# Optimization experiments

Hardware: AMD Instinct MI355X
Metric: run time of the kernel (lower is better)

## Reference

```python
import jax, jax.numpy as jnp
import numpy as np

H = 16      # n_head
DK = 64     # d_k = n_feat // n_head
EPS = 1e-5  # nn.LayerNorm default eps


def _layernorm(x, gamma, beta):
    # LayerNorm over the last (d_k) dim, matching nn.LayerNorm(d_k)
    mu = jnp.mean(x, axis=-1, keepdims=True)
    var = jnp.mean(jnp.square(x - mu), axis=-1, keepdims=True)
    return (x - mu) * jax.lax.rsqrt(var + EPS) * gamma + beta


def setup_inputs() -> dict:
    key = jax.random.key(0)
    ks = jax.random.split(key, 10)
    B, T, D = 4, 1024, 1024
    s = 0.02
    inp = {
        "query": jax.random.normal(ks[0], (B, T, D), dtype=jnp.float32),
        "key":   jax.random.normal(ks[1], (B, T, D), dtype=jnp.float32),
        "value": jax.random.normal(ks[2], (B, T, D), dtype=jnp.float32),
        "mask":  jax.random.randint(ks[3], (B, T, T), 0, 2).astype(bool),
        # projection weights (torch nn.Linear: y = x @ W.T + b)
        "Wq": jax.random.normal(ks[4], (D, D), dtype=jnp.float32) * s,
        "bq": jnp.zeros((D,), dtype=jnp.float32),
        "Wk": jax.random.normal(ks[5], (D, D), dtype=jnp.float32) * s,
        "bk": jnp.zeros((D,), dtype=jnp.float32),
        "Wv": jax.random.normal(ks[6], (D, D), dtype=jnp.float32) * s,
        "bv": jnp.zeros((D,), dtype=jnp.float32),
        "Wo": jax.random.normal(ks[7], (D, D), dtype=jnp.float32) * s,
        "bo": jnp.zeros((D,), dtype=jnp.float32),
        # per-head LayerNorm params over d_k
        "q_gamma": jnp.ones((DK,), dtype=jnp.float32),
        "q_beta":  jnp.zeros((DK,), dtype=jnp.float32),
        "k_gamma": jnp.ones((DK,), dtype=jnp.float32),
        "k_beta":  jnp.zeros((DK,), dtype=jnp.float32),
    }
    return inp


def reference(query, key, value, mask, Wq, bq, Wk, bk, Wv, bv, Wo, bo,
              q_gamma, q_beta, k_gamma, k_beta):
    B, Tq, D = query.shape
    Tk = key.shape[1]
    # forward_qkv: project, split heads, QK-LayerNorm
    q = (query @ Wq.T + bq).reshape(B, Tq, H, DK)
    k = (key   @ Wk.T + bk).reshape(B, Tk, H, DK)
    q = _layernorm(q, q_gamma, q_beta).transpose(0, 2, 1, 3)  # (B,H,Tq,dk)
    k = _layernorm(k, k_gamma, k_beta).transpose(0, 2, 1, 3)  # (B,H,Tk,dk)
    v = (value @ Wv.T + bv).reshape(B, Tk, H, DK).transpose(0, 2, 1, 3)
    # scores scaled by sqrt(d_k)
    scores = jnp.einsum('bhqd,bhkd->bhqk', q, k) / jnp.sqrt(jnp.float32(DK))
    m = mask[:, None]  # (B,1,Tq,Tk) broadcast over heads
    scores = jnp.where(m, jnp.float32(-10000.0), scores)
    attn = jax.nn.softmax(scores, axis=-1)
    attn = jnp.where(m, jnp.float32(0.0), attn)
    # dropout is identity (p=0.0, eval)
    x = jnp.einsum('bhqk,bhkd->bhqd', attn, v)
    x = x.transpose(0, 2, 1, 3).reshape(B, Tq, H * DK)
    return x @ Wo.T + bo
```

## Files before the change

kernel.cpp:

```cpp
#include <hip/hip_runtime.h>
#include <cstdint>
#include <cstddef>

typedef _Float16 half8  __attribute__((ext_vector_type(8)));
typedef _Float16 half4v __attribute__((ext_vector_type(4)));
typedef float    f32x4  __attribute__((ext_vector_type(4)));

__device__ __forceinline__ f32x4 fzero4() {
  f32x4 v; v[0] = v[1] = v[2] = v[3] = 0.0f; return v;
}

__device__ __forceinline__ void gload16(const void* g, void* l) {
  __builtin_amdgcn_global_load_lds(
      (const __attribute__((address_space(1))) unsigned int*)g,
      (__attribute__((address_space(3))) unsigned int*)l, 16, 0, 0);
}

#define MFMA(a, b, c) __builtin_amdgcn_mfma_f32_16x16x32_f16(a, b, c, 0, 0, 0)
#define EXP2(x) __builtin_amdgcn_exp2f(x)

__device__ __forceinline__ float row16_sum(float x) {
#define STEP_(N)                                                         \
  {                                                                      \
    int t_ = __builtin_amdgcn_update_dpp(0, __float_as_int(x), 0x120 | N, \
                                         0xf, 0xf, true);                \
    x = x + __int_as_float(t_);                                          \
  }
  STEP_(8) STEP_(4) STEP_(2) STEP_(1)
#undef STEP_
  return x;
}

struct PrepArgs {
  const float* src[7];
  _Float16*    dst[7];
  const int*   mask;
  unsigned long long* mbits;
};

__global__ __launch_bounds__(256) void prep_kernel(PrepArgs a) {
  const int z = blockIdx.y;
  const int nthr = gridDim.x * blockDim.x;
  const int t0 = blockIdx.x * blockDim.x + threadIdx.x;
  if (z < 3) {
    const float4* __restrict__ s = (const float4*)a.src[z];
    half4v* __restrict__ d = (half4v*)a.dst[z];
    float4 v[8];
#pragma unroll
    for (int k = 0; k < 8; ++k) v[k] = s[t0 + k * nthr];
#pragma unroll
    for (int k = 0; k < 8; ++k) {
      half4v h;
      h[0] = (_Float16)v[k].x; h[1] = (_Float16)v[k].y;
      h[2] = (_Float16)v[k].z; h[3] = (_Float16)v[k].w;
      d[t0 + k * nthr] = h;
    }
  } else if (z < 7) {
    const float4* __restrict__ s = (const float4*)a.src[z];
    half4v* __restrict__ d = (half4v*)a.dst[z];
    float4 v[2];
#pragma unroll
    for (int k = 0; k < 2; ++k) v[k] = s[t0 + k * nthr];
#pragma unroll
    for (int k = 0; k < 2; ++k) {
      half4v h;
      h[0] = (_Float16)v[k].x; h[1] = (_Float16)v[k].y;
      h[2] = (_Float16)v[k].z; h[3] = (_Float16)v[k].w;
      d[t0 + k * nthr] = h;
    }
  } else {
    const int* __restrict__ src = a.mask;
    const unsigned char* __restrict__ s8 = (const unsigned char*)src;
    unsigned long long* __restrict__ dst = a.mbits;
    const int lane = threadIdx.x & 63;
    unsigned probe = 0;
#pragma unroll
    for (int e = 0; e < 16; ++e) probe |= s8[4 * (lane * 16 + e) + 1];
    const bool isbool = __any(probe != 0);

    const int gw = blockIdx.x * 4 + (threadIdx.x >> 6);
    for (int ii = 0; ii < 32; ii += 8) {
      int mv[8];
#pragma unroll
      for (int k = 0; k < 8; ++k) {
        const int word = gw * 32 + ii + k;
        const int t = word & 1023;
        const int kw = (word >> 10) & 15;
        const int b = word >> 14;
        const size_t idx = ((size_t)(b * 1024 + t)) * 1024 + kw * 64 + lane;
        mv[k] = isbool ? (int)s8[idx] : src[idx];
      }
#pragma unroll
      for (int k = 0; k < 8; ++k) {
        unsigned long long bal = __ballot(mv[k] != 0);
        if (lane == 0) dst[gw * 32 + ii + k] = bal;
      }
    }
  }
}

#define SM_SCALE 0.18033688011112042f

__global__ __launch_bounds__(256) void proj_kernel(
    const _Float16* __restrict__ q16, const _Float16* __restrict__ k16,
    const _Float16* __restrict__ v16, const _Float16* __restrict__ w16,
    const float* __restrict__ bq, const float* __restrict__ bk,
    const float* __restrict__ bv,
    const float* __restrict__ qg, const float* __restrict__ qbt,
    const float* __restrict__ kg, const float* __restrict__ kbt,
    _Float16* __restrict__ Qln, _Float16* __restrict__ Kln,
    _Float16* __restrict__ VT) {
  __shared__ _Float16 As[128 * 64];
  __shared__ _Float16 Bs[128 * 64];

  const int tid = threadIdx.x;
  const int w = tid >> 6, lane = tid & 63, g = lane >> 4, l15 = lane & 15;
  const int flat = blockIdx.x;
  const int swz = (flat & 7) * 96 + (flat >> 3);
  const int bn = swz & 7;
  const int bm = (swz >> 3) & 31;
  const int z = swz >> 8;

  const _Float16* A = (z == 0) ? q16 : ((z == 1) ? k16 : v16);
  const _Float16* W = w16 + (size_t)z * (1024 * 1024);
  const float* bias = (z == 0) ? bq : ((z == 1) ? bk : bv);

  const int wr = w >> 1, wc = w & 1;
  const int srow = (w << 3) + (lane >> 3);
  const int csw = ((lane & 7) ^ (lane >> 3)) << 3;
  const int rsw = (l15 & 7) << 3;

  f32x4 acc[4][4];
#pragma unroll
  for (int i = 0; i < 4; ++i)
#pragma unroll
    for (int j = 0; j < 4; ++j) acc[i][j] = fzero4();

#define PROJ_STAGE(KT)                                                      \
  _Pragma("unroll") for (int r = 0; r < 4; ++r) {                           \
    const int row = r * 32 + srow;                                          \
    gload16(A + (size_t)(bm * 128 + row) * 1024 + (KT)*64 + csw,            \
            &As[(r * 32 + (w << 3)) * 64]);                                 \
    gload16(W + (size_t)(bn * 128 + row) * 1024 + (KT)*64 + csw,            \
            &Bs[(r * 32 + (w << 3)) * 64]);                                 \
  }

#define PROJ_COMP()                                                         \
  _Pragma("unroll") for (int kk = 0; kk < 2; ++kk) {                        \
    half8 a[4], b[4];                                                       \
    _Pragma("unroll") for (int mi = 0; mi < 4; ++mi) a[mi] =                \
        *(const half8*)&As[(wr * 64 + mi * 16 + l15) * 64 +                 \
                           ((kk * 32 + g * 8) ^ rsw)];                      \
    _Pragma("unroll") for (int nj = 0; nj < 4; ++nj) b[nj] =                \
        *(const half8*)&Bs[(wc * 64 + nj * 16 + l15) * 64 +                 \
                           ((kk * 32 + g * 8) ^ rsw)];                      \
    __builtin_amdgcn_s_setprio(1);                                          \
    _Pragma("unroll") for (int mi = 0; mi < 4; ++mi)                        \
        _Pragma("unroll") for (int nj = 0; nj < 4; ++nj) acc[mi][nj] =      \
            MFMA(a[mi], b[nj], acc[mi][nj]);                                \
    __builtin_amdgcn_s_setprio(0);                                          \
  }

  for (int kt = 0; kt < 16; ++kt) {
    PROJ_STAGE(kt)
    asm volatile("s_waitcnt vmcnt(0)" ::: "memory");
    __syncthreads();
    PROJ_COMP()
    __syncthreads();
  }
#undef PROJ_COMP
#undef PROJ_STAGE

  const int colbase = bn * 128 + wc * 64;
  const int h = colbase >> 6;
  const int rowbase = bm * 128 + wr * 64;

  float biasv[4];
#pragma unroll
  for (int nj = 0; nj < 4; ++nj) biasv[nj] = bias[colbase + nj * 16 + l15];

  if (z < 2) {
    const float* gamma = (z == 0) ? qg : kg;
    const float* beta = (z == 0) ? qbt : kbt;
    const float sc = (z == 0) ? SM_SCALE : 1.0f;
    _Float16* dst = (z == 0) ? Qln : Kln;
    float gam[4], bet[4];
#pragma unroll
    for (int nj = 0; nj < 4; ++nj) {
      gam[nj] = gamma[nj * 16 + l15] * sc;
      bet[nj] = beta[nj * 16 + l15] * sc;
    }
#pragma unroll
    for (int mi = 0; mi < 4; ++mi) {
#pragma unroll
      for (int j = 0; j < 4; ++j) {
        float vals[4], s = 0.f, s2 = 0.f;
#pragma unroll
        for (int nj = 0; nj < 4; ++nj) {
          float v = acc[mi][nj][j] + biasv[nj];
          vals[nj] = v; s += v; s2 += v * v;
        }
        s = row16_sum(s);
        s2 = row16_sum(s2);
        const float mu = s * (1.0f / 64.0f);
        const float var = s2 * (1.0f / 64.0f) - mu * mu;
        const float rs = rsqrtf(var + 1e-5f);
        const int r = rowbase + mi * 16 + g * 4 + j;
        const int b = r >> 10, t = r & 1023;
        _Float16* drow = dst + ((size_t)((b * 16 + h) * 1024 + t)) * 64;
#pragma unroll
        for (int nj = 0; nj < 4; ++nj)
          drow[nj * 16 + l15] =
              (_Float16)((vals[nj] - mu) * rs * gam[nj] + bet[nj]);
      }
    }
  } else {
#pragma unroll
    for (int mi = 0; mi < 4; ++mi) {
      const int r0 = rowbase + mi * 16 + g * 4;
      const int b = r0 >> 10, t0 = r0 & 1023;
#pragma unroll
      for (int nj = 0; nj < 4; ++nj) {
        const int dk = nj * 16 + l15;
        half4v pk;
#pragma unroll
        for (int j = 0; j < 4; ++j)
          pk[j] = (_Float16)(acc[mi][nj][j] + biasv[nj]);
        *(half4v*)&VT[((size_t)((b * 16 + h) * 64 + dk)) * 1024 + t0] = pk;
      }
    }
  }
}

#define PSTR 76

__global__ __launch_bounds__(512) void attn_kernel(
    const _Float16* __restrict__ Qln, const _Float16* __restrict__ Kln,
    const _Float16* __restrict__ VT,
    const unsigned long long* __restrict__ mbits, _Float16* __restrict__ X) {
  __shared__ _Float16 PQ[128 * PSTR];
  __shared__ _Float16 Ks[2][64 * 64];
  __shared__ _Float16 Vs[2][64 * 64];
  __shared__ unsigned long long Mb[2][128];

  const int tid = threadIdx.x;
  const int w = tid >> 6, lane = tid & 63, g = lane >> 4, l15 = lane & 15;
  const int qt = blockIdx.y;
  const int bh = blockIdx.x;
  const int b = bh >> 4, h = bh & 15;

  const int lr8 = lane >> 3;
  const int csw = ((lane & 7) ^ lr8) << 3;

  const _Float16* Qb = Qln + (size_t)bh * 65536;
  const _Float16* Kb = Kln + (size_t)bh * 65536;
  const _Float16* Vb = VT + (size_t)bh * 65536;
  const unsigned long long* mbb = mbits + (size_t)b * 16384 + qt * 128;

  gload16(Qb + (size_t)(qt * 128 + w * 16 + lr8) * 64 + csw, &PQ[(w * 16) * 64]);
  gload16(Qb + (size_t)(qt * 128 + w * 16 + 8 + lr8) * 64 + csw,
          &PQ[(w * 16 + 8) * 64]);
  gload16(Kb + (size_t)(w * 8 + lr8) * 64 + csw, &Ks[0][(w * 8) * 64]);
  gload16(Vb + (size_t)(w * 8 + lr8) * 1024 + csw, &Vs[0][(w * 8) * 64]);
  if (w == 0) gload16(mbb + lane * 2, &Mb[0][0]);
  asm volatile("s_waitcnt vmcnt(0)" ::: "memory");
  __syncthreads();

  const int rsw = (l15 & 7) << 3;
  half8 qf[2];
#pragma unroll
  for (int kk = 0; kk < 2; ++kk)
    qf[kk] = *(const half8*)&PQ[(w * 16 + l15) * 64 + ((kk * 32 + g * 8) ^ rsw)];
  asm volatile("s_waitcnt lgkmcnt(0)" ::: "memory");
  __syncthreads();

  f32x4 o[4];
  float lsum[4];
#pragma unroll
  for (int dn = 0; dn < 4; ++dn) o[dn] = fzero4();
#pragma unroll
  for (int j = 0; j < 4; ++j) lsum[j] = 0.f;

#define ATTN_TILE(KT, CUR, NXT, PF)                                          \
  {                                                                          \
    if (PF) {                                                                \
      gload16(Kb + (size_t)(((KT) + 1) * 64 + w * 8 + lr8) * 64 + csw,       \
              &Ks[NXT][(w * 8) * 64]);                                       \
      gload16(Vb + (size_t)(w * 8 + lr8) * 1024 + ((KT) + 1) * 64 + csw,     \
              &Vs[NXT][(w * 8) * 64]);                                       \
      if (w == 0)                                                            \
        gload16(mbb + (size_t)((KT) + 1) * 1024 + lane * 2, &Mb[NXT][0]);    \
    }                                                                        \
    f32x4 s[4];                                                              \
    _Pragma("unroll") for (int nj = 0; nj < 4; ++nj) s[nj] = fzero4();       \
    _Pragma("unroll") for (int kk = 0; kk < 2; ++kk) {                       \
      half8 qv = qf[kk];                                                     \
      __builtin_amdgcn_s_setprio(1);                                         \
      _Pragma("unroll") for (int nj = 0; nj < 4; ++nj) {                     \
        half8 kf = *(const half8*)&Ks[CUR][(nj * 16 + l15) * 64 +            \
                                          ((kk * 32 + g * 8) ^ rsw)];        \
        s[nj] = MFMA(qv, kf, s[nj]);                                         \
      }                                                                      \
      __builtin_amdgcn_s_setprio(0);                                         \
    }                                                                        \
    _Pragma("unroll") for (int j = 0; j < 4; ++j) {                          \
      const int lrow = w * 16 + g * 4 + j;                                   \
      const unsigned long long mw = Mb[CUR][lrow];                           \
      const unsigned lo = (unsigned)mw, hi = (unsigned)(mw >> 32);           \
      const float p0 = ((lo >> l15) & 1) ? 0.f : EXP2(s[0][j]);              \
      const float p1 = ((lo >> (l15 + 16)) & 1) ? 0.f : EXP2(s[1][j]);       \
      const float p2 = ((hi >> l15) & 1) ? 0.f : EXP2(s[2][j]);              \
      const float p3 = ((hi >> (l15 + 16)) & 1) ? 0.f : EXP2(s[3][j]);       \
      PQ[lrow * PSTR + 0 + l15] = (_Float16)p0;                              \
      PQ[lrow * PSTR + 16 + l15] = (_Float16)p1;                             \
      PQ[lrow * PSTR + 32 + l15] = (_Float16)p2;                             \
      PQ[lrow * PSTR + 48 + l15] = (_Float16)p3;                             \
      lsum[j] += (p0 + p1) + (p2 + p3);                                      \
    }                                                                        \
    _Pragma("unroll") for (int kk = 0; kk < 2; ++kk) {                       \
      half8 pa = *(const half8*)&PQ[(w * 16 + l15) * PSTR + kk * 32 + g * 8];\
      __builtin_amdgcn_s_setprio(1);                                         \
      _Pragma("unroll") for (int dn = 0; dn < 4; ++dn) {                     \
        half8 vf = *(const half8*)&Vs[CUR][(dn * 16 + l15) * 64 +            \
                                           ((kk * 32 + g * 8) ^ rsw)];       \
        o[dn] = MFMA(pa, vf, o[dn]);                                         \
      }                                                                      \
      __builtin_amdgcn_s_setprio(0);                                         \
    }                                                                        \
    if (PF) {                                                                \
      asm volatile("s_waitcnt vmcnt(0)" ::: "memory");                       \
      __syncthreads();                                                       \
    }                                                                        \
  }

  for (int kt = 0; kt < 16; kt += 2) {
    ATTN_TILE(kt, 0, 1, true);
    ATTN_TILE(kt + 1, 1, 0, (kt + 1) < 15);
  }
#undef ATTN_TILE

#pragma unroll
  for (int j = 0; j < 4; ++j) {
    const int t = qt * 128 + w * 16 + g * 4 + j;
    const float inv = 1.0f / row16_sum(lsum[j]);
    _Float16* xrow = X + ((size_t)(b * 1024 + t)) * 1024 + h * 64;
#pragma unroll
    for (int dn = 0; dn < 4; ++dn)
      xrow[dn * 16 + l15] = (_Float16)(o[dn][j] * inv);
  }
}

__global__ __launch_bounds__(256) void ogemm_kernel(
    const _Float16* __restrict__ Xin, const _Float16* __restrict__ Wo16,
    const float* __restrict__ bo, float* __restrict__ out) {
  __shared__ _Float16 As[2][128 * 64];
  __shared__ _Float16 Bs[2][64 * 64];

  const int tid = threadIdx.x;
  const int w = tid >> 6, lane = tid & 63, g = lane >> 4, l15 = lane & 15;
  const int flat = blockIdx.x;
  const int swz = (flat & 7) * 64 + (flat >> 3);
  const int bn = swz & 15;
  const int bm = swz >> 4;
  const int wr = w >> 1, wc = w & 1;
  const int srow = (w << 3) + (lane >> 3);
  const int lr8 = lane >> 3;
  const int csw = ((lane & 7) ^ lr8) << 3;
  const int rsw = (l15 & 7) << 3;

  f32x4 acc[4][2];
#pragma unroll
  for (int i = 0; i < 4; ++i)
#pragma unroll
    for (int j = 0; j < 2; ++j) acc[i][j] = fzero4();

#define OG_STAGE(KT, BUF)                                                   \
  {                                                                         \
    _Pragma("unroll") for (int r = 0; r < 4; ++r) {                         \
      gload16(Xin + (size_t)(bm * 128 + r * 32 + srow) * 1024 + (KT)*64 +   \
                  csw,                                                      \
              &As[BUF][(r * 32 + (w << 3)) * 64]);                          \
    }                                                                       \
    _Pragma("unroll") for (int c = 0; c < 2; ++c) {                         \
      gload16(Wo16 + (size_t)(bn * 64 + w * 16 + c * 8 + lr8) * 1024 +      \
                  (KT)*64 + csw,                                            \
              &Bs[BUF][(w * 16 + c * 8) * 64]);                             \
    }                                                                       \
  }

#define OG_TILE(KT, CUR, NXT, PF)                                           \
  {                                                                         \
    if (PF) { OG_STAGE((KT) + 1, NXT) }                                     \
    _Pragma("unroll") for (int kk = 0; kk < 2; ++kk) {                      \
      half8 a[4], b[2];                                                     \
      _Pragma("unroll") for (int mi = 0; mi < 4; ++mi) a[mi] =              \
          *(const half8*)&As[CUR][(wr * 64 + mi * 16 + l15) * 64 +          \
                                  ((kk * 32 + g * 8) ^ rsw)];               \
      _Pragma("unroll") for (int nj = 0; nj < 2; ++nj) b[nj] =              \
          *(const half8*)&Bs[CUR][(wc * 32 + nj * 16 + l15) * 64 +          \
                                  ((kk * 32 + g * 8) ^ rsw)];               \
      __builtin_amdgcn_s_setprio(1);                                        \
      _Pragma("unroll") for (int mi = 0; mi < 4; ++mi)                      \
          _Pragma("unroll") for (int nj = 0; nj < 2; ++nj) acc[mi][nj] =    \
              MFMA(a[mi], b[nj], acc[mi][nj]);                              \
      __builtin_amdgcn_s_setprio(0);                                        \
    }                                                                       \
    if (PF) {                                                               \
      asm volatile("s_waitcnt vmcnt(0)" ::: "memory");                      \
      __syncthreads();                                                      \
    }                                                                       \
  }

  OG_STAGE(0, 0)
  asm volatile("s_waitcnt vmcnt(0)" ::: "memory");
  __syncthreads();
  for (int kt = 0; kt < 16; kt += 2) {
    OG_TILE(kt, 0, 1, true);
    OG_TILE(kt + 1, 1, 0, (kt + 1) < 15);
  }
#undef OG_TILE
#undef OG_STAGE

  const int colbase = bn * 64 + wc * 32;
  const int rowbase = bm * 128 + wr * 64;
  float biasv[2];
#pragma unroll
  for (int nj = 0; nj < 2; ++nj) biasv[nj] = bo[colbase + nj * 16 + l15];
#pragma unroll
  for (int mi = 0; mi < 4; ++mi)
#pragma unroll
    for (int nj = 0; nj < 2; ++nj)
#pragma unroll
      for (int j = 0; j < 4; ++j) {
        const int r = rowbase + mi * 16 + g * 4 + j;
        out[(size_t)r * 1024 + colbase + nj * 16 + l15] =
            acc[mi][nj][j] + biasv[nj];
      }
}

extern "C" void kernel_launch(void* const* d_in, const int* in_sizes, int n_in,
                              void* d_out, int out_size, void* d_ws,
                              size_t ws_size, hipStream_t stream) {
  const float* query = (const float*)d_in[0];
  const float* key = (const float*)d_in[1];
  const float* value = (const float*)d_in[2];
  const int* mask = (const int*)d_in[3];
  const float* Wq = (const float*)d_in[4];
  const float* bq = (const float*)d_in[5];
  const float* Wk = (const float*)d_in[6];
  const float* bk = (const float*)d_in[7];
  const float* Wv = (const float*)d_in[8];
  const float* bv = (const float*)d_in[9];
  const float* Wo = (const float*)d_in[10];
  const float* bo = (const float*)d_in[11];
  const float* qg = (const float*)d_in[12];
  const float* qb = (const float*)d_in[13];
  const float* kg = (const float*)d_in[14];
  const float* kb = (const float*)d_in[15];
  float* out = (float*)d_out;

  const size_t M4 = (size_t)4 * 1024 * 1024;
  const size_t M1 = (size_t)1024 * 1024;
  _Float16* q16 = (_Float16*)d_ws;
  _Float16* k16 = q16 + M4;
  _Float16* v16 = k16 + M4;
  _Float16* w16 = v16 + M4;
  _Float16* Qln = w16 + M4;
  _Float16* Kln = Qln + M4;
  _Float16* VTp = Kln + M4;
  _Float16* X = q16;
  unsigned long long* mbits = (unsigned long long*)(VTp + M4);

  PrepArgs pa;
  pa.src[0] = query; pa.src[1] = key; pa.src[2] = value;
  pa.src[3] = Wq; pa.src[4] = Wk; pa.src[5] = Wv; pa.src[6] = Wo;
  pa.dst[0] = q16; pa.dst[1] = k16; pa.dst[2] = v16;
  pa.dst[3] = w16; pa.dst[4] = w16 + M1; pa.dst[5] = w16 + 2 * M1;
  pa.dst[6] = w16 + 3 * M1;
  pa.mask = mask;
  pa.mbits = mbits;

  prep_kernel<<<dim3(512, 8), 256, 0, stream>>>(pa);
  proj_kernel<<<dim3(768), 256, 0, stream>>>(
      q16, k16, v16, w16, bq, bk, bv, qg, qb, kg, kb, Qln, Kln, VTp);
  attn_kernel<<<dim3(64, 8), 512, 0, stream>>>(Qln, Kln, VTp, mbits, X);
  ogemm_kernel<<<dim3(512), 256, 0, stream>>>(X, w16 + 3 * M1, bo, out);
}
```

Before: 116.2 us.

## Repack mask bitmask with int4 loads and interleaved per-row bit layout

The mask-packing path now reads the int32 mask with 16-byte vector loads and emits four ballot words per 256-column group, which interleaves column bits (lane*4+c) in the packed layout. The attention kernel changes its mask staging to match: it loads four 64-bit words per row once every four key tiles into a larger double-buffered LDS array and decodes bits with a new index formula. This is meant to make the mask-packing reads coalesced and cheaper, in exchange for more LDS space for mask words and more index arithmetic in the softmax loop.

```diff
diff --git a/kernel.cpp b/kernel.cpp
--- a/kernel.cpp
+++ b/kernel.cpp
@@ -78,22 +78,38 @@
     for (int e = 0; e < 16; ++e) probe |= s8[4 * (lane * 16 + e) + 1];
     const bool isbool = __any(probe != 0);
 
-    const int gw = blockIdx.x * 4 + (threadIdx.x >> 6);
-    for (int ii = 0; ii < 32; ii += 8) {
-      int mv[8];
-#pragma unroll
-      for (int k = 0; k < 8; ++k) {
-        const int word = gw * 32 + ii + k;
-        const int t = word & 1023;
-        const int kw = (word >> 10) & 15;
-        const int b = word >> 14;
-        const size_t idx = ((size_t)(b * 1024 + t)) * 1024 + kw * 64 + lane;
-        mv[k] = isbool ? (int)s8[idx] : src[idx];
+    const int wv = blockIdx.x * 4 + (threadIdx.x >> 6);
+    if (!isbool) {
+      const int4* __restrict__ s4 = (const int4*)src;
+      int4 mv[8];
+#pragma unroll
+      for (int i = 0; i < 8; ++i) {
+        const int unit = wv * 8 + i;
+        const int row = unit >> 2, kg = unit & 3;
+        mv[i] = s4[row * 256 + kg * 64 + lane];
       }
 #pragma unroll
-      for (int k = 0; k < 8; ++k) {
-        unsigned long long bal = __ballot(mv[k] != 0);
-        if (lane == 0) dst[gw * 32 + ii + k] = bal;
+      for (int i = 0; i < 8; ++i) {
+        const int unit = wv * 8 + i;
+        unsigned long long w0 = __ballot(mv[i].x != 0);
+        unsigned long long w1 = __ballot(mv[i].y != 0);
+        unsigned long long w2 = __ballot(mv[i].z != 0);
+        unsigned long long w3 = __ballot(mv[i].w != 0);
+        if (lane == 0) {
+          unsigned long long* p = dst + (size_t)unit * 4;
+          p[0] = w0; p[1] = w1; p[2] = w2; p[3] = w3;
+        }
+      }
+    } else {
+      for (int i = 0; i < 8; ++i) {
+        const int unit = wv * 8 + i;
+        const int row = unit >> 2, kg = unit & 3;
+#pragma unroll
+        for (int c = 0; c < 4; ++c) {
+          int m = s8[(size_t)row * 1024 + kg * 256 + lane * 4 + c];
+          unsigned long long bw = __ballot(m != 0);
+          if (lane == 0) dst[(size_t)unit * 4 + c] = bw;
+        }
       }
     }
   }
@@ -241,7 +257,7 @@
   __shared__ _Float16 PQ[128 * PSTR];
   __shared__ _Float16 Ks[2][64 * 64];
   __shared__ _Float16 Vs[2][64 * 64];
-  __shared__ unsigned long long Mb[2][128];
+  __shared__ unsigned long long Mb2[2][128 * 4];
 
   const int tid = threadIdx.x;
   const int w = tid >> 6, lane = tid & 63, g = lane >> 4, l15 = lane & 15;
@@ -255,14 +271,20 @@
   const _Float16* Qb = Qln + (size_t)bh * 65536;
   const _Float16* Kb = Kln + (size_t)bh * 65536;
   const _Float16* Vb = VT + (size_t)bh * 65536;
-  const unsigned long long* mbb = mbits + (size_t)b * 16384 + qt * 128;
+  const unsigned long long* mbb = mbits + (size_t)b * 16384;
+
+#define MB_STAGE(M, BUF)                                                     \
+  if (w < 4)                                                                 \
+    gload16(mbb + (size_t)(qt * 128 + w * 32 + (lane >> 1)) * 16 + (M)*4 +   \
+                (lane & 1) * 2,                                              \
+            &Mb2[BUF][(w * 32) * 4]);
 
   gload16(Qb + (size_t)(qt * 128 + w * 16 + lr8) * 64 + csw, &PQ[(w * 16) * 64]);
   gload16(Qb + (size_t)(qt * 128 + w * 16 + 8 + lr8) * 64 + csw,
           &PQ[(w * 16 + 8) * 64]);
   gload16(Kb + (size_t)(w * 8 + lr8) * 64 + csw, &Ks[0][(w * 8) * 64]);
   gload16(Vb + (size_t)(w * 8 + lr8) * 1024 + csw, &Vs[0][(w * 8) * 64]);
-  if (w == 0) gload16(mbb + lane * 2, &Mb[0][0]);
+  MB_STAGE(0, 0)
   asm volatile("s_waitcnt vmcnt(0)" ::: "memory");
   __syncthreads();
 
@@ -288,8 +310,9 @@
               &Ks[NXT][(w * 8) * 64]);                                       \
       gload16(Vb + (size_t)(w * 8 + lr8) * 1024 + ((KT) + 1) * 64 + csw,     \
               &Vs[NXT][(w * 8) * 64]);                                       \
-      if (w == 0)                                                            \
-        gload16(mbb + (size_t)((KT) + 1) * 1024 + lane * 2, &Mb[NXT][0]);    \
+    }                                                                        \
+    if ((((KT) & 3) == 0) && (((KT) >> 2) < 3)) {                            \
+      MB_STAGE(((KT) >> 2) + 1, (((KT) >> 2) + 1) & 1)                       \
     }                                                                        \
     f32x4 s[4];                                                              \
     _Pragma("unroll") for (int nj = 0; nj < 4; ++nj) s[nj] = fzero4();       \
@@ -305,12 +328,13 @@
     }                                                                        \
     _Pragma("unroll") for (int j = 0; j < 4; ++j) {                          \
       const int lrow = w * 16 + g * 4 + j;                                   \
-      const unsigned long long mw = Mb[CUR][lrow];                           \
-      const unsigned lo = (unsigned)mw, hi = (unsigned)(mw >> 32);           \
-      const float p0 = ((lo >> l15) & 1) ? 0.f : EXP2(s[0][j]);              \
-      const float p1 = ((lo >> (l15 + 16)) & 1) ? 0.f : EXP2(s[1][j]);       \
-      const float p2 = ((hi >> l15) & 1) ? 0.f : EXP2(s[2][j]);              \
-      const float p3 = ((hi >> (l15 + 16)) & 1) ? 0.f : EXP2(s[3][j]);       \
+      const unsigned long long mw =                                          \
+          Mb2[((KT) >> 2) & 1][lrow * 4 + (l15 & 3)];                        \
+      const int bb = ((KT) & 3) * 16 + (l15 >> 2);                           \
+      const float p0 = ((mw >> bb) & 1) ? 0.f : EXP2(s[0][j]);               \
+      const float p1 = ((mw >> (bb + 4)) & 1) ? 0.f : EXP2(s[1][j]);         \
+      const float p2 = ((mw >> (bb + 8)) & 1) ? 0.f : EXP2(s[2][j]);         \
+      const float p3 = ((mw >> (bb + 12)) & 1) ? 0.f : EXP2(s[3][j]);        \
       PQ[lrow * PSTR + 0 + l15] = (_Float16)p0;                              \
       PQ[lrow * PSTR + 16 + l15] = (_Float16)p1;                             \
       PQ[lrow * PSTR + 32 + l15] = (_Float16)p2;                             \
@@ -338,6 +362,7 @@
     ATTN_TILE(kt + 1, 1, 0, (kt + 1) < 15);
   }
 #undef ATTN_TILE
+#undef MB_STAGE
 
 #pragma unroll
   for (int j = 0; j < 4; ++j) {
```

Result: no change. 115.4 us (-0.7%).
